# Kernel tuning notes

Hardware: AMD Instinct MI355X
Metric: run time of the kernel (lower is better)

## Reference

```python
import jax, jax.numpy as jnp
import numpy as np

# Dims derived from the module: len(vocab)=V, E=V-4, bidirectional 2-layer LSTM.
V, E, H, L = 1028, 1024, 1024, 2
B, T = 16, 512
BOS, PAD = 1, 0  # vocab.bos_idx, vocab.pad_idx


def setup_inputs() -> dict:
    key = jax.random.key(0)
    ks = jax.random.split(key, 10)
    sc = 1.0 / np.sqrt(H)  # PyTorch LSTM init scale
    inputs = jax.random.randint(ks[0], (B, T), 0, V, dtype=jnp.int32)
    emb = (jax.random.normal(ks[1], (V, E), jnp.float32) * 0.02).at[PAD].set(0.0)
    # [dir, 4H, in_dim] weights; layer 0 consumes E, layer 1 consumes 2H (bidir concat).
    w_ih_l0 = jax.random.uniform(ks[2], (2, 4 * H, E), jnp.float32, -sc, sc)
    w_hh_l0 = jax.random.uniform(ks[3], (2, 4 * H, H), jnp.float32, -sc, sc)
    b_ih_l0 = jax.random.uniform(ks[4], (2, 4 * H), jnp.float32, -sc, sc)
    b_hh_l0 = jax.random.uniform(ks[5], (2, 4 * H), jnp.float32, -sc, sc)
    w_ih_l1 = jax.random.uniform(ks[6], (2, 4 * H, 2 * H), jnp.float32, -sc, sc)
    w_hh_l1 = jax.random.uniform(ks[7], (2, 4 * H, H), jnp.float32, -sc, sc)
    b_ih_l1 = jax.random.uniform(ks[8], (2, 4 * H), jnp.float32, -sc, sc)
    b_hh_l1 = jax.random.uniform(ks[9], (2, 4 * H), jnp.float32, -sc, sc)
    return {"inputs": inputs, "emb": emb,
            "w_ih_l0": w_ih_l0, "w_hh_l0": w_hh_l0, "b_ih_l0": b_ih_l0, "b_hh_l0": b_hh_l0,
            "w_ih_l1": w_ih_l1, "w_hh_l1": w_hh_l1, "b_ih_l1": b_ih_l1, "b_hh_l1": b_hh_l1}


def lstm_cell(x, h, c, wih, whh, b):
    # PyTorch gate order: i, f, g, o
    g = x @ wih.T + h @ whh.T + b
    i, f, gg, o = jnp.split(g, 4, axis=-1)
    c2 = jax.nn.sigmoid(f) * c + jax.nn.sigmoid(i) * jnp.tanh(gg)
    h2 = jax.nn.sigmoid(o) * jnp.tanh(c2)
    return h2, c2


def reference(inputs, emb, w_ih_l0, w_hh_l0, b_ih_l0, b_hh_l0,
              w_ih_l1, w_hh_l1, b_ih_l1, b_hh_l1):
    Bb, Tt = inputs.shape
    # step 0 consumes BOS; steps i>=1 consume inputs[:, i] (inputs[:,0] is never used)
    toks = jnp.concatenate([jnp.full((Bb, 1), BOS, inputs.dtype), inputs[:, 1:]], axis=1)
    xs = emb[toks].transpose(1, 0, 2)  # [T, B, E]; dropout is eval-mode identity
    b0 = b_ih_l0 + b_hh_l0
    b1 = b_ih_l1 + b_hh_l1
    h0 = jnp.zeros((4, Bb, H), xs.dtype)  # [l0f, l0b, l1f, l1b]
    c0 = jnp.zeros((4, Bb, H), xs.dtype)

    def step(carry, x):
        h, c = carry
        # length-1 sequence: forward and backward directions see the same token
        h0f, c0f = lstm_cell(x, h[0], c[0], w_ih_l0[0], w_hh_l0[0], b0[0])
        h0b, c0b = lstm_cell(x, h[1], c[1], w_ih_l0[1], w_hh_l0[1], b0[1])
        x1 = jnp.concatenate([h0f, h0b], axis=-1)  # [B, 2H]
        h1f, c1f = lstm_cell(x1, h[2], c[2], w_ih_l1[0], w_hh_l1[0], b1[0])
        h1b, c1b = lstm_cell(x1, h[3], c[3], w_ih_l1[1], w_hh_l1[1], b1[1])
        out = jnp.concatenate([h1f, h1b], axis=-1)  # [B, 2H]
        return (jnp.stack([h0f, h0b, h1f, h1b]), jnp.stack([c0f, c0b, c1f, c1b])), out

    _, outs = jax.lax.scan(step, (h0, c0), xs)
    return outs.transpose(1, 0, 2)  # [B, T, 2H]
```

## Files before the change

kernel.cpp:

```cpp
#include <hip/hip_runtime.h>
#include <hip/hip_bf16.h>
#include <stdint.h>


#define TT 512
#define HH 1024

typedef __bf16 bf16x8 __attribute__((ext_vector_type(8)));
typedef float f32x4 __attribute__((ext_vector_type(4)));
typedef unsigned int u32;
typedef unsigned short u16;

#define MFMA __builtin_amdgcn_mfma_f32_16x16x32_bf16

#define OFS_FLAGS 0ul
#define OFS_B0    4096ul
#define OFS_B1    36864ul
#define OFS_X     69632ul
#define OFS_WIH0  16846848ul
#define OFS_WHH0  33624064ul
#define OFS_W1    50401280ul
#define OFS_H0    100732928ul
#define OFS_H1    134287360ul

__device__ inline u16 f2b(float f){
  union { float f; u32 u; } x{f};
  return (u16)((x.u + 0x7FFFu + ((x.u >> 16) & 1u)) >> 16);
}
__device__ inline float sigm(float x){ return 1.f/(1.f + __expf(-x)); }
__device__ inline float tanh_(float x){ return 2.f*sigm(2.f*x) - 1.f; }

__device__ inline u32 g_poll1(const u32* p){
  u32 v;
  asm volatile("global_load_dword %0, %1, off sc0 sc1\n\t"
               "s_waitcnt vmcnt(0)" : "=&v"(v) : "v"(p) : "memory");
  return v;
}
__device__ inline void g_poll2(const u32* p, const u32* q, u32& a, u32& b){
  asm volatile("global_load_dword %0, %2, off sc0 sc1\n\t"
               "global_load_dword %1, %3, off sc0 sc1\n\t"
               "s_waitcnt vmcnt(0)"
               : "=&v"(a), "=&v"(b) : "v"(p), "v"(q) : "memory");
}
__device__ inline void g_store32(u32* p, u32 v){
  asm volatile("global_store_dword %0, %1, off sc0 sc1" :: "v"(p), "v"(v) : "memory");
}

#define G_LOAD4_ISSUE(A, P) asm volatile( \
  "global_load_dwordx4 %0, %4, off sc0 sc1\n\t" \
  "global_load_dwordx4 %1, %4, off offset:64 sc0 sc1\n\t" \
  "global_load_dwordx4 %2, %4, off offset:128 sc0 sc1\n\t" \
  "global_load_dwordx4 %3, %4, off offset:192 sc0 sc1" \
  : "=&v"(A[0]), "=&v"(A[1]), "=&v"(A[2]), "=&v"(A[3]) \
  : "v"(P) : "memory")
#define G_WAIT0() asm volatile("s_waitcnt vmcnt(0)" ::: "memory")

__global__ void k_bias(const float* __restrict__ a0, const float* __restrict__ a1,
                       const float* __restrict__ a2, const float* __restrict__ a3,
                       float* __restrict__ b0, float* __restrict__ b1,
                       unsigned long long* __restrict__ h1z){
  int i = blockIdx.x*256 + threadIdx.x;
  if (i < 8192){ b0[i] = a0[i] + a1[i]; b1[i] = a2[i] + a3[i]; h1z[i] = 0ull; }
}

__global__ void k_embed(const int* __restrict__ inputs, const float* __restrict__ emb,
                        u16* __restrict__ X){
  int row = blockIdx.x;
  int t = row >> 4, b = row & 15;
  int tok = (t == 0) ? 1 : inputs[b*TT + t];
  const float4* src = (const float4*)(emb + (size_t)tok*HH);
  float4 v = src[threadIdx.x];
  ushort4 o = make_ushort4(f2b(v.x), f2b(v.y), f2b(v.z), f2b(v.w));
  ((ushort4*)X)[(size_t)row*256 + threadIdx.x] = o;
}

__global__ void k_pack(const float* __restrict__ sA, const float* __restrict__ sB,
                       int KA, int KB, u16* __restrict__ dst){
  int K = KA + KB, KS = K >> 5;
  long idx = (long)blockIdx.x*256 + threadIdx.x;
  long total = 2L*64*4*KS*64;
  if (idx >= total) return;
  int l = (int)(idx & 63);
  long r = idx >> 6;
  int ks = (int)(r % KS); r /= KS;
  int g  = (int)(r & 3);  r >>= 2;
  int jb = (int)(r & 63); r >>= 6;
  int cell = (int)r;
  int n  = g*1024 + jb*16 + (l & 15);
  int k0 = ks*32 + ((l >> 4) << 3);
  const float* s; int kl;
  if (k0 < KA){ s = sA + (long)(cell*4096 + n)*KA; kl = k0; }
  else        { s = sB + (long)(cell*4096 + n)*KB; kl = k0 - KA; }
  float4 f0 = *(const float4*)(s + kl);
  float4 f1 = *(const float4*)(s + kl + 4);
  union { u16 v[8]; int4 q; } o;
  o.v[0]=f2b(f0.x); o.v[1]=f2b(f0.y); o.v[2]=f2b(f0.z); o.v[3]=f2b(f0.w);
  o.v[4]=f2b(f1.x); o.v[5]=f2b(f1.y); o.v[6]=f2b(f1.z); o.v[7]=f2b(f1.w);
  long d = ((((long)cell*64 + jb)*4 + g)*KS + ks)*64 + l;
  ((int4*)dst)[d] = o.q;
}

__global__ __launch_bounds__(512, 2)
void k_fused(const u16* __restrict__ Wih0p, const u16* __restrict__ Whh0p,
             const u16* __restrict__ W1p, const float* __restrict__ b0,
             const float* __restrict__ b1, const u16* __restrict__ Xb,
             u16* h0_all, u16* h1r, float* __restrict__ out, u32* flags)
{
  extern __shared__ char smem[];
  float*  gl   = (float*)smem;
  f32x4*  wlds = (f32x4*)(smem + 32768);

  const int tid  = threadIdx.x;
  const int wv   = tid >> 6, l = tid & 63;
  const int rowA = l & 15;
  const int kq8  = (l >> 4) * 8;
  const int layer = blockIdx.x >> 7;
  const int bid   = blockIdx.x & 127;
  const int cell  = bid >> 6, jb = bid & 63;
  const int b_ = tid >> 4, j = tid & 15;

  float bias[4];
  {
    const float* bb = (layer == 0 ? b0 : b1) + cell*4096 + jb*16 + rowA;
    #pragma unroll
    for (int g = 0; g < 4; g++) bias[g] = (wv == 0) ? bb[g*1024] : 0.f;
  }
  float creg = 0.f;

  if (layer == 0){
    f32x4 w[4][8];
    {
      const f32x4* src = (const f32x4*)(wv < 4 ? Wih0p : Whh0p)
                       + ((long)(cell*64 + jb)*4)*32*64 + l;
      #pragma unroll
      for (int g = 0; g < 4; g++)
        #pragma unroll
        for (int i = 0; i < 8; i++)
          w[g][i] = src[((long)g*32 + (wv & 3)*8 + i)*64];
    }
    #pragma unroll
    for (int g = 0; g < 4; g++)
      #pragma unroll
      for (int i = 0; i < 8; i++) asm volatile("" : "+v"(w[g][i]));
    __syncthreads();

    const u32* flr = flags + cell*64;
    u32* myf = flags + cell*64 + jb;
    u32* hdst = (u32*)h0_all;
    const int ko = (wv & 3)*256;

    for (int t = 0; t < TT; t++){
      f32x4 acc[4];
      #pragma unroll
      for (int g = 0; g < 4; g++) acc[g] = (f32x4){bias[g],bias[g],bias[g],bias[g]};
      if (wv < 4){
        const u16* A = Xb + ((long)t*16 + rowA)*1024 + ko + kq8;
        f32x4 Af[8];
        #pragma unroll
        for (int i = 0; i < 8; i++) Af[i] = *(const f32x4*)(A + i*32);
        #pragma unroll
        for (int i = 0; i < 8; i++)
          #pragma unroll
          for (int g = 0; g < 4; g++)
            acc[g] = MFMA(__builtin_bit_cast(bf16x8, Af[i]),
                          __builtin_bit_cast(bf16x8, w[g][i]), acc[g], 0, 0, 0);
        int r0 = (l >> 4)*4, cj = l & 15;
        #pragma unroll
        for (int g = 0; g < 4; g++)
          #pragma unroll
          for (int i2 = 0; i2 < 4; i2++)
            gl[wv*1024 + g*256 + (r0+i2)*16 + cj] = acc[g][i2];
      } else if (wv == 7 && t > 0){
        while (!__all((int)(g_poll1(flr + l) >= (u32)t))) {}
      }
      __syncthreads();
      if (wv >= 4){
        if (t > 0){
          const u16* A = h0_all + (((long)(t-1)*2 + cell)*16 + rowA)*1024 + ko + kq8;
          f32x4 Af[8];
          #pragma unroll
          for (int i = 0; i < 8; i++) Af[i] = *(const f32x4*)(A + i*32);
          #pragma unroll
          for (int i = 0; i < 8; i++)
            #pragma unroll
            for (int g = 0; g < 4; g++)
              acc[g] = MFMA(__builtin_bit_cast(bf16x8, Af[i]),
                            __builtin_bit_cast(bf16x8, w[g][i]), acc[g], 0, 0, 0);
        }
        int r0 = (l >> 4)*4, cj = l & 15;
        #pragma unroll
        for (int g = 0; g < 4; g++)
          #pragma unroll
          for (int i2 = 0; i2 < 4; i2++)
            gl[wv*1024 + g*256 + (r0+i2)*16 + cj] = acc[g][i2];
      }
      __syncthreads();
      if (tid < 256){
        float s0=0.f, s1=0.f, s2=0.f, s3=0.f;
        #pragma unroll
        for (int wq = 0; wq < 8; wq++){
          s0 += gl[wq*1024 + tid];
          s1 += gl[wq*1024 + 256 + tid];
          s2 += gl[wq*1024 + 512 + tid];
          s3 += gl[wq*1024 + 768 + tid];
        }
        float c2 = sigm(s1)*creg + sigm(s0)*tanh_(s2);
        float h2 = sigm(s3)*tanh_(c2);
        creg = c2;
        u32 lo = f2b(h2), hi = __shfl_down(lo, 1);
        if (!(tid & 1)){
          long idx = ((((long)t*2 + cell)*16 + b_)*1024 + jb*16 + j) >> 1;
          g_store32(hdst + idx, lo | (hi << 16));
        }
        G_WAIT0();
      }
      __syncthreads();
      if (tid == 0) g_store32(myf, (u32)(t+1));
    }
  } else {
    f32x4 wh0[4][8];
    f32x4 wh1[4];
    {
      const f32x4* src = (const f32x4*)W1p + ((long)(cell*64 + jb)*4)*96*64 + l;
      #pragma unroll
      for (int g = 0; g < 4; g++){
        #pragma unroll
        for (int i = 0; i < 8; i++)
          wh0[g][i] = src[((long)g*96 + wv*8 + i)*64];
        wh1[g] = src[((long)g*96 + 64 + wv*4)*64];
      }
      const f32x4* wb = (const f32x4*)W1p + ((long)(cell*64 + jb)*4)*96*64;
      for (int i = tid; i < 6144; i += 512){
        int g = i / 1536, r = (i % 1536) >> 6, ll = i & 63;
        int ksl = 64 + (r/3)*4 + (r%3) + 1;
        wlds[i] = wb[((long)g*96 + ksl)*64 + ll];
      }
    }
    #pragma unroll
    for (int g = 0; g < 4; g++){
      #pragma unroll
      for (int i = 0; i < 8; i++) asm volatile("" : "+v"(wh0[g][i]));
      asm volatile("" : "+v"(wh1[g]));
    }
    __syncthreads();

    const u32* fl0 = flags;
    const u32* fl1 = flags + 64;
    const u32* flo = flags + (2 + cell)*64;
    u32* myf = flags + (2 + cell)*64 + jb;
    u32* h1d = (u32*)h1r;

    for (int t = 0; t < TT; t++){
      if (wv == 7){
        const u32 tgt = (u32)(t + 1);
        for (;;){
          u32 a, b; g_poll2(fl0 + l, fl1 + l, a, b);
          if (__all((int)(a >= tgt && b >= tgt))) break;
        }
      } else if (wv == 6 && t > 0){
        while (!__all((int)(g_poll1(flo + l) >= (u32)t))) {}
      }
      __syncthreads();
      f32x4 acc[4];
      #pragma unroll
      for (int g = 0; g < 4; g++) acc[g] = (f32x4){bias[g],bias[g],bias[g],bias[g]};
      f32x4 Bf[4];
      {
        const u16* Ah = h1r + (((long)((t+3)&3)*2 + cell)*16 + rowA)*1024
                      + wv*128 + kq8;
        G_LOAD4_ISSUE(Bf, Ah);
      }
      {
        const u16* A = h0_all + ((long)t*32 + (wv>>2)*16 + rowA)*1024
                     + (wv & 3)*256 + kq8;
        f32x4 Af[8];
        #pragma unroll
        for (int i = 0; i < 8; i++) Af[i] = *(const f32x4*)(A + i*32);
        #pragma unroll
        for (int i = 0; i < 8; i++)
          #pragma unroll
          for (int g = 0; g < 4; g++)
            acc[g] = MFMA(__builtin_bit_cast(bf16x8, Af[i]),
                          __builtin_bit_cast(bf16x8, wh0[g][i]), acc[g], 0, 0, 0);
      }
      G_WAIT0();
      #pragma unroll
      for (int i = 0; i < 4; i++)
        #pragma unroll
        for (int g = 0; g < 4; g++){
          f32x4 bw = (i == 0) ? wh1[g] : wlds[(g*24 + wv*3 + (i-1))*64 + l];
          acc[g] = MFMA(__builtin_bit_cast(bf16x8, Bf[i]),
                        __builtin_bit_cast(bf16x8, bw), acc[g], 0, 0, 0);
        }
      {
        int r0 = (l >> 4)*4, cj = l & 15;
        #pragma unroll
        for (int g = 0; g < 4; g++)
          #pragma unroll
          for (int i2 = 0; i2 < 4; i2++)
            gl[wv*1024 + g*256 + (r0+i2)*16 + cj] = acc[g][i2];
      }
      __syncthreads();
      if (tid < 256){
        float s0=0.f, s1=0.f, s2=0.f, s3=0.f;
        #pragma unroll
        for (int wq = 0; wq < 8; wq++){
          s0 += gl[wq*1024 + tid];
          s1 += gl[wq*1024 + 256 + tid];
          s2 += gl[wq*1024 + 512 + tid];
          s3 += gl[wq*1024 + 768 + tid];
        }
        float c2 = sigm(s1)*creg + sigm(s0)*tanh_(s2);
        float h2 = sigm(s3)*tanh_(c2);
        creg = c2;
        out[((long)b_*TT + t)*2048 + cell*1024 + jb*16 + j] = h2;
        u32 lo = f2b(h2), hi = __shfl_down(lo, 1);
        if (!(tid & 1)){
          long idx = ((((long)(t & 3)*2 + cell)*16 + b_)*1024 + jb*16 + j) >> 1;
          g_store32(h1d + idx, lo | (hi << 16));
        }
        G_WAIT0();
      }
      __syncthreads();
      if (tid == 0) g_store32(myf, (u32)(t+1));
    }
  }
}

extern "C" void kernel_launch(void* const* d_in, const int* in_sizes, int n_in,
                              void* d_out, int out_size, void* d_ws, size_t ws_size,
                              hipStream_t stream){
  const int*   inputs = (const int*)d_in[0];
  const float* emb    = (const float*)d_in[1];
  const float* wih0   = (const float*)d_in[2];
  const float* whh0   = (const float*)d_in[3];
  const float* bih0   = (const float*)d_in[4];
  const float* bhh0   = (const float*)d_in[5];
  const float* wih1   = (const float*)d_in[6];
  const float* whh1   = (const float*)d_in[7];
  const float* bih1   = (const float*)d_in[8];
  const float* bhh1   = (const float*)d_in[9];
  float* out = (float*)d_out;
  char* ws = (char*)d_ws;

  u32*   flags = (u32*)(ws + OFS_FLAGS);
  float* b0    = (float*)(ws + OFS_B0);
  float* b1    = (float*)(ws + OFS_B1);
  u16*   Xb    = (u16*)(ws + OFS_X);
  u16*   Wih0p = (u16*)(ws + OFS_WIH0);
  u16*   Whh0p = (u16*)(ws + OFS_WHH0);
  u16*   W1p   = (u16*)(ws + OFS_W1);
  u16*   h0a   = (u16*)(ws + OFS_H0);
  u16*   h1r   = (u16*)(ws + OFS_H1);
  unsigned long long* h1z = (unsigned long long*)(ws + OFS_H1 + 196608ul);

  hipMemsetAsync(flags, 0, 4096, stream);
  k_bias <<<32,   256, 0, stream>>>(bih0, bhh0, bih1, bhh1, b0, b1, h1z);
  k_embed<<<8192, 256, 0, stream>>>(inputs, emb, Xb);
  k_pack <<<4096, 256, 0, stream>>>(wih0, (const float*)0, 1024, 0, Wih0p);
  k_pack <<<4096, 256, 0, stream>>>(whh0, (const float*)0, 1024, 0, Whh0p);
  k_pack <<<12288,256, 0, stream>>>(wih1, whh1, 2048, 1024, W1p);

  const int smem_bytes = 32768 + 98304;
  hipFuncSetAttribute(reinterpret_cast<const void*>(&k_fused),
                      hipFuncAttributeMaxDynamicSharedMemorySize, smem_bytes);
  k_fused<<<256, 512, smem_bytes, stream>>>(Wih0p, Whh0p, W1p, b0, b1, Xb,
                                            h0a, h1r, out, flags);
}
```

Baseline: 3.734 ms.

## Replace flag-based inter-block sync with sentinel-valued data polling

```diff
diff --git a/kernel.cpp b/kernel.cpp
--- a/kernel.cpp
+++ b/kernel.cpp
@@ -13,7 +13,6 @@
 
 #define MFMA __builtin_amdgcn_mfma_f32_16x16x32_bf16
 
-#define OFS_FLAGS 0ul
 #define OFS_B0    4096ul
 #define OFS_B1    36864ul
 #define OFS_X     69632ul
@@ -30,21 +29,23 @@
 __device__ inline float sigm(float x){ return 1.f/(1.f + __expf(-x)); }
 __device__ inline float tanh_(float x){ return 2.f*sigm(2.f*x) - 1.f; }
 
-__device__ inline u32 g_poll1(const u32* p){
-  u32 v;
-  asm volatile("global_load_dword %0, %1, off sc0 sc1\n\t"
-               "s_waitcnt vmcnt(0)" : "=&v"(v) : "v"(p) : "memory");
-  return v;
-}
-__device__ inline void g_poll2(const u32* p, const u32* q, u32& a, u32& b){
-  asm volatile("global_load_dword %0, %2, off sc0 sc1\n\t"
-               "global_load_dword %1, %3, off sc0 sc1\n\t"
-               "s_waitcnt vmcnt(0)"
-               : "=&v"(a), "=&v"(b) : "v"(p), "v"(q) : "memory");
-}
 __device__ inline void g_store32(u32* p, u32 v){
   asm volatile("global_store_dword %0, %1, off sc0 sc1" :: "v"(p), "v"(v) : "memory");
 }
+
+#define G_LOAD8(A, P) asm volatile( \
+  "global_load_dwordx4 %0, %8, off sc0 sc1\n\t" \
+  "global_load_dwordx4 %1, %8, off offset:64 sc0 sc1\n\t" \
+  "global_load_dwordx4 %2, %8, off offset:128 sc0 sc1\n\t" \
+  "global_load_dwordx4 %3, %8, off offset:192 sc0 sc1\n\t" \
+  "global_load_dwordx4 %4, %8, off offset:256 sc0 sc1\n\t" \
+  "global_load_dwordx4 %5, %8, off offset:320 sc0 sc1\n\t" \
+  "global_load_dwordx4 %6, %8, off offset:384 sc0 sc1\n\t" \
+  "global_load_dwordx4 %7, %8, off offset:448 sc0 sc1\n\t" \
+  "s_waitcnt vmcnt(0)" \
+  : "=&v"(A[0]), "=&v"(A[1]), "=&v"(A[2]), "=&v"(A[3]), \
+    "=&v"(A[4]), "=&v"(A[5]), "=&v"(A[6]), "=&v"(A[7]) \
+  : "v"(P) : "memory")
 
 #define G_LOAD4_ISSUE(A, P) asm volatile( \
   "global_load_dwordx4 %0, %4, off sc0 sc1\n\t" \
@@ -53,7 +54,22 @@
   "global_load_dwordx4 %3, %4, off offset:192 sc0 sc1" \
   : "=&v"(A[0]), "=&v"(A[1]), "=&v"(A[2]), "=&v"(A[3]) \
   : "v"(P) : "memory")
-#define G_WAIT0() asm volatile("s_waitcnt vmcnt(0)" ::: "memory")
+#define G_WAIT4(A) asm volatile("s_waitcnt vmcnt(0)" \
+  : "+v"(A[0]), "+v"(A[1]), "+v"(A[2]), "+v"(A[3]) :: "memory")
+#define G_LOAD4W(A, P) asm volatile( \
+  "global_load_dwordx4 %0, %4, off sc0 sc1\n\t" \
+  "global_load_dwordx4 %1, %4, off offset:64 sc0 sc1\n\t" \
+  "global_load_dwordx4 %2, %4, off offset:128 sc0 sc1\n\t" \
+  "global_load_dwordx4 %3, %4, off offset:192 sc0 sc1\n\t" \
+  "s_waitcnt vmcnt(0)" \
+  : "=&v"(A[0]), "=&v"(A[1]), "=&v"(A[2]), "=&v"(A[3]) \
+  : "v"(P) : "memory")
+
+__device__ inline int frag_ok(const f32x4 v){
+  uint4 u = __builtin_bit_cast(uint4, v);
+  return (u.x != 0xFFFFFFFFu) & (u.y != 0xFFFFFFFFu) &
+         (u.z != 0xFFFFFFFFu) & (u.w != 0xFFFFFFFFu);
+}
 
 __global__ void k_bias(const float* __restrict__ a0, const float* __restrict__ a1,
                        const float* __restrict__ a2, const float* __restrict__ a3,
@@ -104,7 +120,7 @@
 void k_fused(const u16* __restrict__ Wih0p, const u16* __restrict__ Whh0p,
              const u16* __restrict__ W1p, const float* __restrict__ b0,
              const float* __restrict__ b1, const u16* __restrict__ Xb,
-             u16* h0_all, u16* h1r, float* __restrict__ out, u32* flags)
+             u16* h0_all, u16* h1r, float* __restrict__ out)
 {
   extern __shared__ char smem[];
   float*  gl   = (float*)smem;
@@ -144,8 +160,6 @@
       for (int i = 0; i < 8; i++) asm volatile("" : "+v"(w[g][i]));
     __syncthreads();
 
-    const u32* flr = flags + cell*64;
-    u32* myf = flags + cell*64 + jb;
     u32* hdst = (u32*)h0_all;
     const int ko = (wv & 3)*256;
 
@@ -164,29 +178,24 @@
           for (int g = 0; g < 4; g++)
             acc[g] = MFMA(__builtin_bit_cast(bf16x8, Af[i]),
                           __builtin_bit_cast(bf16x8, w[g][i]), acc[g], 0, 0, 0);
-        int r0 = (l >> 4)*4, cj = l & 15;
-        #pragma unroll
-        for (int g = 0; g < 4; g++)
-          #pragma unroll
-          for (int i2 = 0; i2 < 4; i2++)
-            gl[wv*1024 + g*256 + (r0+i2)*16 + cj] = acc[g][i2];
-      } else if (wv == 7 && t > 0){
-        while (!__all((int)(g_poll1(flr + l) >= (u32)t))) {}
-      }
-      __syncthreads();
-      if (wv >= 4){
-        if (t > 0){
-          const u16* A = h0_all + (((long)(t-1)*2 + cell)*16 + rowA)*1024 + ko + kq8;
-          f32x4 Af[8];
-          #pragma unroll
-          for (int i = 0; i < 8; i++) Af[i] = *(const f32x4*)(A + i*32);
-          #pragma unroll
-          for (int i = 0; i < 8; i++)
-            #pragma unroll
-            for (int g = 0; g < 4; g++)
-              acc[g] = MFMA(__builtin_bit_cast(bf16x8, Af[i]),
-                            __builtin_bit_cast(bf16x8, w[g][i]), acc[g], 0, 0, 0);
-        }
+      } else if (t > 0){
+        const u16* A = h0_all + (((long)(t-1)*2 + cell)*16 + rowA)*1024 + ko + kq8;
+        f32x4 Af[8];
+        for (;;){
+          G_LOAD8(Af, A);
+          int ok = 1;
+          #pragma unroll
+          for (int i = 0; i < 8; i++) ok &= frag_ok(Af[i]);
+          if (__all(ok)) break;
+        }
+        #pragma unroll
+        for (int i = 0; i < 8; i++)
+          #pragma unroll
+          for (int g = 0; g < 4; g++)
+            acc[g] = MFMA(__builtin_bit_cast(bf16x8, Af[i]),
+                          __builtin_bit_cast(bf16x8, w[g][i]), acc[g], 0, 0, 0);
+      }
+      {
         int r0 = (l >> 4)*4, cj = l & 15;
         #pragma unroll
         for (int g = 0; g < 4; g++)
@@ -212,10 +221,8 @@
           long idx = ((((long)t*2 + cell)*16 + b_)*1024 + jb*16 + j) >> 1;
           g_store32(hdst + idx, lo | (hi << 16));
         }
-        G_WAIT0();
       }
       __syncthreads();
-      if (tid == 0) g_store32(myf, (u32)(t+1));
     }
   } else {
     f32x4 wh0[4][8];
@@ -244,38 +251,31 @@
     }
     __syncthreads();
 
-    const u32* fl0 = flags;
-    const u32* fl1 = flags + 64;
-    const u32* flo = flags + (2 + cell)*64;
-    u32* myf = flags + (2 + cell)*64 + jb;
     u32* h1d = (u32*)h1r;
 
     for (int t = 0; t < TT; t++){
-      if (wv == 7){
-        const u32 tgt = (u32)(t + 1);
-        for (;;){
-          u32 a, b; g_poll2(fl0 + l, fl1 + l, a, b);
-          if (__all((int)(a >= tgt && b >= tgt))) break;
-        }
-      } else if (wv == 6 && t > 0){
-        while (!__all((int)(g_poll1(flo + l) >= (u32)t))) {}
-      }
-      __syncthreads();
+      if (tid < 256 && !(tid & 1)){
+        long idx = ((((long)((t+1)&3)*2 + cell)*16 + b_)*1024 + jb*16 + j) >> 1;
+        g_store32(h1d + idx, 0xFFFFFFFFu);
+      }
+      f32x4 Bf[4];
+      const u16* Ah = h1r + (((long)((t+3)&3)*2 + cell)*16 + rowA)*1024
+                    + wv*128 + kq8;
+      G_LOAD4_ISSUE(Bf, Ah);
       f32x4 acc[4];
       #pragma unroll
       for (int g = 0; g < 4; g++) acc[g] = (f32x4){bias[g],bias[g],bias[g],bias[g]};
-      f32x4 Bf[4];
-      {
-        const u16* Ah = h1r + (((long)((t+3)&3)*2 + cell)*16 + rowA)*1024
-                      + wv*128 + kq8;
-        G_LOAD4_ISSUE(Bf, Ah);
-      }
       {
         const u16* A = h0_all + ((long)t*32 + (wv>>2)*16 + rowA)*1024
                      + (wv & 3)*256 + kq8;
         f32x4 Af[8];
-        #pragma unroll
-        for (int i = 0; i < 8; i++) Af[i] = *(const f32x4*)(A + i*32);
+        for (;;){
+          G_LOAD8(Af, A);
+          int ok = 1;
+          #pragma unroll
+          for (int i = 0; i < 8; i++) ok &= frag_ok(Af[i]);
+          if (__all(ok)) break;
+        }
         #pragma unroll
         for (int i = 0; i < 8; i++)
           #pragma unroll
@@ -283,7 +283,14 @@
             acc[g] = MFMA(__builtin_bit_cast(bf16x8, Af[i]),
                           __builtin_bit_cast(bf16x8, wh0[g][i]), acc[g], 0, 0, 0);
       }
-      G_WAIT0();
+      G_WAIT4(Bf);
+      for (;;){
+        int ok = 1;
+        #pragma unroll
+        for (int i = 0; i < 4; i++) ok &= frag_ok(Bf[i]);
+        if (__all(ok)) break;
+        G_LOAD4W(Bf, Ah);
+      }
       #pragma unroll
       for (int i = 0; i < 4; i++)
         #pragma unroll
@@ -319,10 +326,8 @@
           long idx = ((((long)(t & 3)*2 + cell)*16 + b_)*1024 + jb*16 + j) >> 1;
           g_store32(h1d + idx, lo | (hi << 16));
         }
-        G_WAIT0();
       }
       __syncthreads();
-      if (tid == 0) g_store32(myf, (u32)(t+1));
     }
   }
 }
@@ -343,7 +348,6 @@
   float* out = (float*)d_out;
   char* ws = (char*)d_ws;
 
-  u32*   flags = (u32*)(ws + OFS_FLAGS);
   float* b0    = (float*)(ws + OFS_B0);
   float* b1    = (float*)(ws + OFS_B1);
   u16*   Xb    = (u16*)(ws + OFS_X);
@@ -354,7 +358,8 @@
   u16*   h1r   = (u16*)(ws + OFS_H1);
   unsigned long long* h1z = (unsigned long long*)(ws + OFS_H1 + 196608ul);
 
-  hipMemsetAsync(flags, 0, 4096, stream);
+  hipMemsetAsync(ws + OFS_H0, 0xFF, 33554432ul, stream);
+  hipMemsetAsync(ws + OFS_H1, 0xFF, 196608ul, stream);
   k_bias <<<32,   256, 0, stream>>>(bih0, bhh0, bih1, bhh1, b0, b1, h1z);
   k_embed<<<8192, 256, 0, stream>>>(inputs, emb, Xb);
   k_pack <<<4096, 256, 0, stream>>>(wih0, (const float*)0, 1024, 0, Wih0p);
@@ -365,5 +370,5 @@
   hipFuncSetAttribute(reinterpret_cast<const void*>(&k_fused),
                       hipFuncAttributeMaxDynamicSharedMemorySize, smem_bytes);
   k_fused<<<256, 512, smem_bytes, stream>>>(Wih0p, Whh0p, W1p, b0, b1, Xb,
-                                            h0a, h1r, out, flags);
-}
+                                            h0a, h1r, out);
+}
```

Measured after the change: 3.043 ms. 18.5% less time.
